# Kernel optimization log

Hardware: AMD Instinct MI355X
Metric: run time of the kernel (lower is better)

The kernel has to match this reference:

```python
import math
import jax, jax.numpy as jnp
import numpy as np

DIM = 1024
N_HEADS = 16
N_KV_HEADS = 4
HEAD_DIM = 64
WINDOW = 512
EPS = 1e-6
B, S = 2, 2048

def _alibi_slopes(n_heads):
    def pow2(n):
        r = 2.0 ** (-8.0 / n)
        return np.array([r ** (i + 1) for i in range(n)], dtype=np.float32)
    if math.log2(n_heads).is_integer():
        return pow2(n_heads)
    m = 2 ** math.floor(math.log2(n_heads))
    return np.concatenate([pow2(m), pow2(2 * m)[::2][: n_heads - m]])

def _rmsnorm(x, w, eps=EPS):
    var = jnp.mean(x * x, axis=-1, keepdims=True)
    return x * jax.lax.rsqrt(var + eps) * w

def setup_inputs() -> dict:
    key = jax.random.key(0)
    ks = jax.random.split(key, 8)
    x = jax.random.normal(ks[0], (B, S, DIM), dtype=jnp.float32)
    wq = 0.02 * jax.random.normal(ks[1], (N_HEADS * HEAD_DIM, DIM), dtype=jnp.float32)
    wk = 0.02 * jax.random.normal(ks[2], (N_KV_HEADS * HEAD_DIM, DIM), dtype=jnp.float32)
    wv = 0.02 * jax.random.normal(ks[3], (N_KV_HEADS * HEAD_DIM, DIM), dtype=jnp.float32)
    wo = 0.02 * jax.random.normal(ks[4], (DIM, N_HEADS * HEAD_DIM), dtype=jnp.float32)
    q_norm_w = jnp.ones((N_HEADS * HEAD_DIM,), dtype=jnp.float32)
    k_norm_w = jnp.ones((N_KV_HEADS * HEAD_DIM,), dtype=jnp.float32)
    return {"x": x, "wq": wq, "wk": wk, "wv": wv, "wo": wo,
            "q_norm_w": q_norm_w, "k_norm_w": k_norm_w}

def reference(x, wq, wk, wv, wo, q_norm_w, k_norm_w):
    bsz, seqlen, _ = x.shape
    repeats = N_HEADS // N_KV_HEADS
    xq = _rmsnorm(x @ wq.T, q_norm_w)
    xk = _rmsnorm(x @ wk.T, k_norm_w)
    xv = x @ wv.T
    # [b, h, s, d]
    q = xq.reshape(bsz, seqlen, N_HEADS, HEAD_DIM).transpose(0, 2, 1, 3)
    k = xk.reshape(bsz, seqlen, N_KV_HEADS, HEAD_DIM).transpose(0, 2, 1, 3)
    v = xv.reshape(bsz, seqlen, N_KV_HEADS, HEAD_DIM).transpose(0, 2, 1, 3)
    k = jnp.repeat(k, repeats, axis=1)
    v = jnp.repeat(v, repeats, axis=1)
    pos = jnp.arange(seqlen)
    rel = pos[None, :] - pos[:, None]  # [s_q, s_k], key - query
    slopes = jnp.asarray(_alibi_slopes(N_HEADS))
    bias = slopes[:, None, None] * rel[None].astype(x.dtype)  # [h, s, s]
    masked = (rel > 0) | (rel < -WINDOW)  # causal + sliding window
    bias = jnp.where(masked[None], -jnp.inf, bias)
    scale = 1.0 / math.sqrt(HEAD_DIM)
    scores = jnp.einsum('bhqd,bhkd->bhqk', q, k) * scale + bias[None]
    probs = jax.nn.softmax(scores, axis=-1)
    y = jnp.einsum('bhqk,bhkd->bhqd', probs, v)
    y = y.transpose(0, 2, 1, 3).reshape(bsz, seqlen, N_HEADS * HEAD_DIM)
    return y @ wo.T
```

## Files before the change

kernel.cpp:

```cpp
#include <hip/hip_runtime.h>

typedef unsigned short u16;
typedef unsigned int u32;

typedef __bf16 bf16x8 __attribute__((ext_vector_type(8)));
typedef float f32x4 __attribute__((ext_vector_type(4)));

__device__ __forceinline__ u16 f2bf(float f) {
  __bf16 h = (__bf16)f;
  return __builtin_bit_cast(u16, h);
}
__device__ __forceinline__ u32 pk2bf(float a, float b) {
  __bf16 lo = (__bf16)a, hi = (__bf16)b;
  return (u32)__builtin_bit_cast(u16, lo) | ((u32)__builtin_bit_cast(u16, hi) << 16);
}
__device__ __forceinline__ float bf2f(u16 v) {
  u32 u = (u32)v << 16;
  return __builtin_bit_cast(float, u);
}

typedef const __attribute__((address_space(1))) u32 gbl_u32;
typedef __attribute__((address_space(3))) u32 lds_u32;
__device__ __forceinline__ void gload_lds16(const u16* g, u16* l) {
  __builtin_amdgcn_global_load_lds((gbl_u32*)g, (lds_u32*)l, 16, 0, 0);
}

__global__ __launch_bounds__(256)
void cvt_all_kernel(const float* __restrict__ x, const float* __restrict__ wq,
                    const float* __restrict__ wk, const float* __restrict__ wv,
                    const float* __restrict__ wo, u16* __restrict__ x_bf,
                    u16* __restrict__ wcat_bf, u16* __restrict__ wo_bf) {
  int t = blockIdx.x * 256 + threadIdx.x;
  const float* src;
  u16* dst;
  if (t < 1048576) {
    src = x; dst = x_bf;
  } else if (t < 1310720) {
    src = wq; dst = wcat_bf; t -= 1048576;
  } else if (t < 1376256) {
    src = wk; dst = wcat_bf + 1048576; t -= 1310720;
  } else if (t < 1441792) {
    src = wv; dst = wcat_bf + 1310720; t -= 1376256;
  } else {
    src = wo; dst = wo_bf; t -= 1441792;
  }
  const int i = t * 4;
  float4 v = *(const float4*)(src + i);
  uint2 p;
  p.x = pk2bf(v.x, v.y);
  p.y = pk2bf(v.z, v.w);
  *(uint2*)(dst + i) = p;
}

template <typename OutT>
__global__ __launch_bounds__(256)
void gemm_bt_kernel(const u16* __restrict__ A, const u16* __restrict__ B,
                    OutT* __restrict__ C, int M, int N, int K) {
  __shared__ u16 As[2][64 * 64];
  __shared__ u16 Bs[2][128 * 64];
  const int tid = threadIdx.x;
  const int lane = tid & 63;
  const int wave = tid >> 6;
  const int wm = (wave >> 1) * 32;
  const int wn = (wave & 1) * 64;
  const int l15 = lane & 15;
  const int quad = lane >> 4;
  const int sw = l15 & 7;
  const size_t bm = (size_t)blockIdx.y * 64;
  const size_t bn = (size_t)blockIdx.x * 128;

  f32x4 acc[2][4];
#pragma unroll
  for (int i = 0; i < 2; ++i)
#pragma unroll
    for (int j = 0; j < 4; ++j) acc[i][j] = f32x4{0.f, 0.f, 0.f, 0.f};

  const int r0 = tid >> 3;
  const int bswz = ((tid & 7) ^ (r0 & 7)) * 8;
  const u16* gA0 = A + (bm + r0) * (size_t)K + bswz;
  const u16* gA1 = A + (bm + r0 + 32) * (size_t)K + bswz;
  const u16* gB0 = B + (bn + r0) * (size_t)K + bswz;
  const u16* gB1 = B + (bn + r0 + 32) * (size_t)K + bswz;
  const u16* gB2 = B + (bn + r0 + 64) * (size_t)K + bswz;
  const u16* gB3 = B + (bn + r0 + 96) * (size_t)K + bswz;

#define STAGE(bufi, kk)                                   \
  do {                                                    \
    gload_lds16(gA0 + (kk), &As[bufi][tid * 8]);          \
    gload_lds16(gA1 + (kk), &As[bufi][2048 + tid * 8]);   \
    gload_lds16(gB0 + (kk), &Bs[bufi][tid * 8]);          \
    gload_lds16(gB1 + (kk), &Bs[bufi][2048 + tid * 8]);   \
    gload_lds16(gB2 + (kk), &Bs[bufi][4096 + tid * 8]);   \
    gload_lds16(gB3 + (kk), &Bs[bufi][6144 + tid * 8]);   \
  } while (0)

  STAGE(0, 0);
  int buf = 0;
  for (int k0 = 0; k0 < K; k0 += 64) {
    __syncthreads();
    if (k0 + 64 < K) STAGE(buf ^ 1, k0 + 64);
    const u16* as = As[buf];
    const u16* bs = Bs[buf];
#pragma unroll
    for (int h = 0; h < 2; ++h) {
      const int cb = quad + 4 * h;
      bf16x8 af[2], bfr[4];
#pragma unroll
      for (int i = 0; i < 2; ++i)
        af[i] = *(const bf16x8*)(&as[(wm + i * 16 + l15) * 64 + ((cb ^ sw) * 8)]);
#pragma unroll
      for (int j = 0; j < 4; ++j)
        bfr[j] = *(const bf16x8*)(&bs[(wn + j * 16 + l15) * 64 + ((cb ^ sw) * 8)]);
#pragma unroll
      for (int i = 0; i < 2; ++i)
#pragma unroll
        for (int j = 0; j < 4; ++j)
          acc[i][j] = __builtin_amdgcn_mfma_f32_16x16x32_bf16(af[i], bfr[j], acc[i][j], 0, 0, 0);
    }
    buf ^= 1;
  }
#undef STAGE

  const int rq = quad * 4;
#pragma unroll
  for (int i = 0; i < 2; ++i) {
#pragma unroll
    for (int r = 0; r < 4; ++r) {
      OutT* crow = C + (bm + wm + i * 16 + rq + r) * (size_t)N + bn + wn + l15;
#pragma unroll
      for (int j = 0; j < 4; ++j) {
        if constexpr (sizeof(OutT) == 2)
          crow[j * 16] = f2bf(acc[i][j][r]);
        else
          crow[j * 16] = acc[i][j][r];
      }
    }
  }
}

__global__ __launch_bounds__(256)
void norm_vtrans_kernel(u16* __restrict__ qkv, const float* __restrict__ qw,
                        const float* __restrict__ kw, u16* __restrict__ vt) {
  __shared__ u16 shmem[64 * 72];
  const int bid = blockIdx.x;
  const int tid = threadIdx.x;
  if (bid < 4096) {
    float* red = (float*)shmem;
    u16* row = qkv + (size_t)bid * 1536;
    uint2 pk = *(const uint2*)(row + tid * 4);
    float v0 = bf2f((u16)pk.x), v1 = bf2f((u16)(pk.x >> 16));
    float v2 = bf2f((u16)pk.y), v3 = bf2f((u16)(pk.y >> 16));
    float ss = v0 * v0 + v1 * v1 + v2 * v2 + v3 * v3;
#pragma unroll
    for (int off = 32; off > 0; off >>= 1) ss += __shfl_down(ss, off);
    if ((tid & 63) == 0) red[tid >> 6] = ss;
    __syncthreads();
    float tot = red[0] + red[1] + red[2] + red[3];
    float rn = rsqrtf(tot * (1.0f / 1024.0f) + 1e-6f);
    float4 w = *(const float4*)(qw + tid * 4);
    uint2 po;
    po.x = pk2bf(v0 * rn * w.x, v1 * rn * w.y);
    po.y = pk2bf(v2 * rn * w.z, v3 * rn * w.w);
    *(uint2*)(row + tid * 4) = po;
    if (tid < 64) {
      uint2 kp = *(const uint2*)(row + 1024 + tid * 4);
      float k0 = bf2f((u16)kp.x), k1 = bf2f((u16)(kp.x >> 16));
      float k2 = bf2f((u16)kp.y), k3 = bf2f((u16)(kp.y >> 16));
      float sk = k0 * k0 + k1 * k1 + k2 * k2 + k3 * k3;
#pragma unroll
      for (int off = 32; off > 0; off >>= 1) sk += __shfl_down(sk, off);
      float tk = __shfl(sk, 0);
      float rk = rsqrtf(tk * (1.0f / 256.0f) + 1e-6f);
      float4 w2 = *(const float4*)(kw + tid * 4);
      uint2 ko;
      ko.x = pk2bf(k0 * rk * w2.x, k1 * rk * w2.y);
      ko.y = pk2bf(k2 * rk * w2.z, k3 * rk * w2.w);
      *(uint2*)(row + 1024 + tid * 4) = ko;
    }
  } else {
    const int e = bid - 4096;
    const int t0 = (e & 31) * 64, kvh = (e >> 5) & 3, b = e >> 7;
    u16(*tile)[72] = (u16(*)[72])shmem;
    const int r = tid >> 2, c16 = (tid & 3) * 16;
    const u16* src = qkv + (size_t)(b * 2048 + t0 + r) * 1536 + 1280 + kvh * 64 + c16;
    *(uint4*)&tile[r][c16] = *(const uint4*)src;
    *(uint4*)&tile[r][c16 + 8] = *(const uint4*)(src + 8);
    __syncthreads();
    const int d = tid >> 2, t16 = (tid & 3) * 16;
    u16 o[16];
#pragma unroll
    for (int j = 0; j < 16; ++j) o[j] = tile[t16 + j][d];
    u16* dst = vt + (size_t)((b * 4 + kvh) * 64 + d) * 2048 + t0 + t16;
    *(uint4*)dst = *(uint4*)&o[0];
    *(uint4*)(dst + 8) = *(uint4*)&o[8];
  }
}

__global__ __launch_bounds__(512)
void attn_kernel(const u16* __restrict__ qkvbf, const u16* __restrict__ vt,
                 u16* __restrict__ ybf) {
  __shared__ u16 Ks[2][64 * 64];
  __shared__ u16 Vts[2][64 * 64];
  __shared__ u16 Ps[128 * 72];
  const int qt = blockIdx.x, h = blockIdx.y, b = blockIdx.z;
  const int kvh = h >> 2, q0 = qt * 128;
  const int tid = threadIdx.x, lane = tid & 63, w = tid >> 6;
  const int l15 = lane & 15, quad = lane >> 4;
  const int swl = l15 & 7;

  const u16* qrow = qkvbf + (size_t)(b * 2048 + q0 + w * 16 + l15) * 1536 + h * 64 + quad * 8;
  const bf16x8 qf0 = *(const bf16x8*)qrow;
  const bf16x8 qf1 = *(const bf16x8*)(qrow + 32);

  const int sr = tid >> 3;
  const int bswz = ((tid & 7) ^ (sr & 7)) * 8;
  const u16* kg = qkvbf + (size_t)(b * 2048 + sr) * 1536 + 1024 + kvh * 64 + bswz;
  const u16* vg = vt + (size_t)((b * 4 + kvh) * 64 + sr) * 2048 + bswz;

#define ASTAGE(bufi, cc)                                          \
  do {                                                            \
    gload_lds16(kg + (size_t)(cc) * 1536, &Ks[bufi][tid * 8]);    \
    gload_lds16(vg + (cc), &Vts[bufi][tid * 8]);                  \
  } while (0)

  f32x4 O[4];
#pragma unroll
  for (int jd = 0; jd < 4; ++jd) O[jd] = f32x4{0.f, 0.f, 0.f, 0.f};
  float m_i = -1e30f, l_i = 0.f;
  const float LOG2E = 1.44269504f;
  const float sc2 = 0.125f * LOG2E;
  const float slope2 = exp2f(-0.5f * (float)(h + 1)) * LOG2E;
  const int c_lo = (q0 >= 512) ? (q0 - 512) : 0;
  const int c_hi = q0 + 64;
  const int myq_lo = q0 + w * 16;
  const int myq_hi = myq_lo + 15;
  const int myq = myq_lo + l15;
  const float srr1 = slope2, srr2 = slope2 * 2.0f, srr3 = slope2 * 3.0f;
  const float si16 = slope2 * 16.0f;

  ASTAGE(0, c_lo);
  int buf = 0;

  for (int c = c_lo; c <= c_hi; c += 64) {
    __syncthreads();
    if (c + 64 <= c_hi) ASTAGE(buf ^ 1, c + 64);

    if (!(c > myq_hi || c + 63 < myq_lo - 512)) {
      f32x4 st[4];
      __builtin_amdgcn_s_setprio(1);
#pragma unroll
      for (int i = 0; i < 4; ++i) {
        const int ro = (i * 16 + l15) * 64;
        bf16x8 a0 = *(const bf16x8*)&Ks[buf][ro + ((quad ^ swl) * 8)];
        bf16x8 a1 = *(const bf16x8*)&Ks[buf][ro + (((4 + quad) ^ swl) * 8)];
        f32x4 z = f32x4{0.f, 0.f, 0.f, 0.f};
        z = __builtin_amdgcn_mfma_f32_16x16x32_bf16(a0, qf0, z, 0, 0, 0);
        st[i] = __builtin_amdgcn_mfma_f32_16x16x32_bf16(a1, qf1, z, 0, 0, 0);
      }
      __builtin_amdgcn_s_setprio(0);

      float sv[4][4];
      float rm = -1e30f;
      const bool interior = (c + 63 <= myq_lo) && (c + 512 >= myq_hi);
      if (interior) {
        float bi = slope2 * (float)(c + quad * 4 - myq);
#pragma unroll
        for (int i = 0; i < 4; ++i) {
          float v0 = fmaf(st[i][0], sc2, bi);
          float v1 = fmaf(st[i][1], sc2, bi + srr1);
          float v2 = fmaf(st[i][2], sc2, bi + srr2);
          float v3 = fmaf(st[i][3], sc2, bi + srr3);
          sv[i][0] = v0; sv[i][1] = v1; sv[i][2] = v2; sv[i][3] = v3;
          rm = fmaxf(fmaxf(fmaxf(rm, v0), fmaxf(v1, v2)), v3);
          bi += si16;
        }
      } else {
#pragma unroll
        for (int i = 0; i < 4; ++i)
#pragma unroll
          for (int r = 0; r < 4; ++r) {
            const int key = c + i * 16 + quad * 4 + r;
            const int rel = key - myq;
            float val = (rel > 0 || rel < -512) ? -1e30f
                                                : fmaf(st[i][r], sc2, slope2 * (float)rel);
            sv[i][r] = val;
            rm = fmaxf(rm, val);
          }
      }
      rm = fmaxf(rm, __shfl_xor(rm, 16));
      rm = fmaxf(rm, __shfl_xor(rm, 32));
      const float mn = fmaxf(m_i, rm);
      const float alpha = exp2f(m_i - mn);
      float ls = 0.f;
#pragma unroll
      for (int i = 0; i < 4; ++i) {
        float p0 = exp2f(sv[i][0] - mn);
        float p1 = exp2f(sv[i][1] - mn);
        float p2 = exp2f(sv[i][2] - mn);
        float p3 = exp2f(sv[i][3] - mn);
        ls += (p0 + p1) + (p2 + p3);
        uint2 pw;
        pw.x = pk2bf(p0, p1);
        pw.y = pk2bf(p2, p3);
        *(uint2*)&Ps[(w * 16 + l15) * 72 + i * 16 + quad * 4] = pw;
      }
      ls += __shfl_xor(ls, 16);
      ls += __shfl_xor(ls, 32);
      l_i = l_i * alpha + ls;
      m_i = mn;

      float ar[4];
#pragma unroll
      for (int r = 0; r < 4; ++r) ar[r] = __shfl(alpha, quad * 4 + r);
#pragma unroll
      for (int jd = 0; jd < 4; ++jd)
#pragma unroll
        for (int r = 0; r < 4; ++r) O[jd][r] *= ar[r];

      bf16x8 pf0 = *(const bf16x8*)&Ps[(w * 16 + l15) * 72 + quad * 8];
      bf16x8 pf1 = *(const bf16x8*)&Ps[(w * 16 + l15) * 72 + 32 + quad * 8];
      __builtin_amdgcn_s_setprio(1);
#pragma unroll
      for (int jd = 0; jd < 4; ++jd) {
        const int ro = (jd * 16 + l15) * 64;
        bf16x8 v0 = *(const bf16x8*)&Vts[buf][ro + ((quad ^ swl) * 8)];
        bf16x8 v1 = *(const bf16x8*)&Vts[buf][ro + (((4 + quad) ^ swl) * 8)];
        O[jd] = __builtin_amdgcn_mfma_f32_16x16x32_bf16(pf0, v0, O[jd], 0, 0, 0);
        O[jd] = __builtin_amdgcn_mfma_f32_16x16x32_bf16(pf1, v1, O[jd], 0, 0, 0);
      }
      __builtin_amdgcn_s_setprio(0);
    }
    buf ^= 1;
  }
#undef ASTAGE

  float lr[4];
#pragma unroll
  for (int r = 0; r < 4; ++r) lr[r] = __shfl(l_i, quad * 4 + r);
#pragma unroll
  for (int r = 0; r < 4; ++r) {
    const float inv = 1.0f / lr[r];
    u16* orow = ybf + (size_t)(b * 2048 + q0 + w * 16 + quad * 4 + r) * 1024 + h * 64 + l15;
#pragma unroll
    for (int jd = 0; jd < 4; ++jd) orow[jd * 16] = f2bf(O[jd][r] * inv);
  }
}

extern "C" void kernel_launch(void* const* d_in, const int* in_sizes, int n_in,
                              void* d_out, int out_size, void* d_ws, size_t ws_size,
                              hipStream_t stream) {
  const float* x = (const float*)d_in[0];
  const float* wq = (const float*)d_in[1];
  const float* wk = (const float*)d_in[2];
  const float* wv = (const float*)d_in[3];
  const float* wo = (const float*)d_in[4];
  const float* qnw = (const float*)d_in[5];
  const float* knw = (const float*)d_in[6];
  float* out = (float*)d_out;
  char* ws = (char*)d_ws;

  u16* x_bf = (u16*)(ws);
  u16* wcat_bf = (u16*)(ws + 8388608);
  u16* wo_bf = (u16*)(ws + 11534336);
  u16* qkv_bf = (u16*)(ws + 13631488);
  u16* vt_bf = (u16*)(ws + 26214400);
  u16* y_bf = (u16*)(ws + 28311552);

  cvt_all_kernel<<<6656, 256, 0, stream>>>(x, wq, wk, wv, wo, x_bf, wcat_bf, wo_bf);

  gemm_bt_kernel<u16><<<dim3(12, 64), 256, 0, stream>>>(x_bf, wcat_bf, qkv_bf, 4096, 1536, 1024);
  norm_vtrans_kernel<<<4352, 256, 0, stream>>>(qkv_bf, qnw, knw, vt_bf);
  attn_kernel<<<dim3(16, 16, 2), 512, 0, stream>>>(qkv_bf, vt_bf, y_bf);
  gemm_bt_kernel<float><<<dim3(8, 64), 256, 0, stream>>>(y_bf, wo_bf, out, 4096, 1024, 1024);
}
```

Baseline: 155.0 us.

## Use a 128x128 single-buffered GEMM tile for the QKV projection

Adds a new GEMM kernel that computes a 128x128 output tile per block, with each wave owning a 64x64 sub-tile, and uses it for the QKV projection in place of the 64x128 double-buffered kernel. Larger tiles raise operand reuse from shared memory and halve the number of blocks. The new kernel gives up double buffering: it loads, synchronizes, then computes each K-step, so global-load latency is no longer overlapped, and the 384 blocks may underfill the GPU's CUs. The other edits are variable renames with no effect.

```diff
diff --git a/kernel.cpp b/kernel.cpp
--- a/kernel.cpp
+++ b/kernel.cpp
@@ -54,6 +54,86 @@
 
 template <typename OutT>
 __global__ __launch_bounds__(256)
+void gemm128_kernel(const u16* __restrict__ A, const u16* __restrict__ B,
+                    OutT* __restrict__ C, int N, int K) {
+  __shared__ u16 As[128 * 64];
+  __shared__ u16 Bs[128 * 64];
+  const int tid = threadIdx.x;
+  const int lane = tid & 63;
+  const int wave = tid >> 6;
+  const int wm = (wave & 1) * 64;
+  const int wn = (wave >> 1) * 64;
+  const int l15 = lane & 15;
+  const int quad = lane >> 4;
+  const int sw = l15 & 7;
+  const size_t bm = (size_t)blockIdx.y * 128;
+  const size_t bn = (size_t)blockIdx.x * 128;
+
+  f32x4 acc[4][4];
+#pragma unroll
+  for (int i = 0; i < 4; ++i)
+#pragma unroll
+    for (int j = 0; j < 4; ++j) acc[i][j] = f32x4{0.f, 0.f, 0.f, 0.f};
+
+  const int r0 = tid >> 3;
+  const int bswz = ((tid & 7) ^ (r0 & 7)) * 8;
+  const u16* gA0 = A + (bm + r0) * (size_t)K + bswz;
+  const u16* gA1 = A + (bm + r0 + 32) * (size_t)K + bswz;
+  const u16* gA2 = A + (bm + r0 + 64) * (size_t)K + bswz;
+  const u16* gA3 = A + (bm + r0 + 96) * (size_t)K + bswz;
+  const u16* gB0 = B + (bn + r0) * (size_t)K + bswz;
+  const u16* gB1 = B + (bn + r0 + 32) * (size_t)K + bswz;
+  const u16* gB2 = B + (bn + r0 + 64) * (size_t)K + bswz;
+  const u16* gB3 = B + (bn + r0 + 96) * (size_t)K + bswz;
+
+  for (int k0 = 0; k0 < K; k0 += 64) {
+    __syncthreads();
+    gload_lds16(gA0 + k0, &As[tid * 8]);
+    gload_lds16(gA1 + k0, &As[2048 + tid * 8]);
+    gload_lds16(gA2 + k0, &As[4096 + tid * 8]);
+    gload_lds16(gA3 + k0, &As[6144 + tid * 8]);
+    gload_lds16(gB0 + k0, &Bs[tid * 8]);
+    gload_lds16(gB1 + k0, &Bs[2048 + tid * 8]);
+    gload_lds16(gB2 + k0, &Bs[4096 + tid * 8]);
+    gload_lds16(gB3 + k0, &Bs[6144 + tid * 8]);
+    __syncthreads();
+#pragma unroll
+    for (int h = 0; h < 2; ++h) {
+      const int cb = quad + 4 * h;
+      bf16x8 af[4], bfr[4];
+#pragma unroll
+      for (int i = 0; i < 4; ++i)
+        af[i] = *(const bf16x8*)(&As[(wm + i * 16 + l15) * 64 + ((cb ^ sw) * 8)]);
+#pragma unroll
+      for (int j = 0; j < 4; ++j)
+        bfr[j] = *(const bf16x8*)(&Bs[(wn + j * 16 + l15) * 64 + ((cb ^ sw) * 8)]);
+#pragma unroll
+      for (int i = 0; i < 4; ++i)
+#pragma unroll
+        for (int j = 0; j < 4; ++j)
+          acc[i][j] = __builtin_amdgcn_mfma_f32_16x16x32_bf16(af[i], bfr[j], acc[i][j], 0, 0, 0);
+    }
+  }
+
+  const int rq = quad * 4;
+#pragma unroll
+  for (int i = 0; i < 4; ++i) {
+#pragma unroll
+    for (int r = 0; r < 4; ++r) {
+      OutT* crow = C + (bm + wm + i * 16 + rq + r) * (size_t)N + bn + wn + l15;
+#pragma unroll
+      for (int j = 0; j < 4; ++j) {
+        if constexpr (sizeof(OutT) == 2)
+          crow[j * 16] = f2bf(acc[i][j][r]);
+        else
+          crow[j * 16] = acc[i][j][r];
+      }
+    }
+  }
+}
+
+template <typename OutT>
+__global__ __launch_bounds__(256)
 void gemm_bt_kernel(const u16* __restrict__ A, const u16* __restrict__ B,
                     OutT* __restrict__ C, int M, int N, int K) {
   __shared__ u16 As[2][64 * 64];
@@ -84,21 +164,21 @@
   const u16* gB2 = B + (bn + r0 + 64) * (size_t)K + bswz;
   const u16* gB3 = B + (bn + r0 + 96) * (size_t)K + bswz;
 
-#define STAGE(bufi, kk)                                   \
-  do {                                                    \
-    gload_lds16(gA0 + (kk), &As[bufi][tid * 8]);          \
-    gload_lds16(gA1 + (kk), &As[bufi][2048 + tid * 8]);   \
-    gload_lds16(gB0 + (kk), &Bs[bufi][tid * 8]);          \
-    gload_lds16(gB1 + (kk), &Bs[bufi][2048 + tid * 8]);   \
-    gload_lds16(gB2 + (kk), &Bs[bufi][4096 + tid * 8]);   \
-    gload_lds16(gB3 + (kk), &Bs[bufi][6144 + tid * 8]);   \
+#define FSTAGE(bufi, kk)                                    \
+  do {                                                      \
+    gload_lds16(gA0 + (kk), &As[bufi][tid * 8]);            \
+    gload_lds16(gA1 + (kk), &As[bufi][2048 + tid * 8]);     \
+    gload_lds16(gB0 + (kk), &Bs[bufi][tid * 8]);            \
+    gload_lds16(gB1 + (kk), &Bs[bufi][2048 + tid * 8]);     \
+    gload_lds16(gB2 + (kk), &Bs[bufi][4096 + tid * 8]);     \
+    gload_lds16(gB3 + (kk), &Bs[bufi][6144 + tid * 8]);     \
   } while (0)
 
-  STAGE(0, 0);
+  FSTAGE(0, 0);
   int buf = 0;
   for (int k0 = 0; k0 < K; k0 += 64) {
     __syncthreads();
-    if (k0 + 64 < K) STAGE(buf ^ 1, k0 + 64);
+    if (k0 + 64 < K) FSTAGE(buf ^ 1, k0 + 64);
     const u16* as = As[buf];
     const u16* bs = Bs[buf];
 #pragma unroll
@@ -119,7 +199,7 @@
     }
     buf ^= 1;
   }
-#undef STAGE
+#undef FSTAGE
 
   const int rq = quad * 4;
 #pragma unroll
@@ -266,12 +346,12 @@
         float bi = slope2 * (float)(c + quad * 4 - myq);
 #pragma unroll
         for (int i = 0; i < 4; ++i) {
-          float v0 = fmaf(st[i][0], sc2, bi);
-          float v1 = fmaf(st[i][1], sc2, bi + srr1);
-          float v2 = fmaf(st[i][2], sc2, bi + srr2);
-          float v3 = fmaf(st[i][3], sc2, bi + srr3);
-          sv[i][0] = v0; sv[i][1] = v1; sv[i][2] = v2; sv[i][3] = v3;
-          rm = fmaxf(fmaxf(fmaxf(rm, v0), fmaxf(v1, v2)), v3);
+          float x0 = fmaf(st[i][0], sc2, bi);
+          float x1 = fmaf(st[i][1], sc2, bi + srr1);
+          float x2 = fmaf(st[i][2], sc2, bi + srr2);
+          float x3 = fmaf(st[i][3], sc2, bi + srr3);
+          sv[i][0] = x0; sv[i][1] = x1; sv[i][2] = x2; sv[i][3] = x3;
+          rm = fmaxf(fmaxf(fmaxf(rm, x0), fmaxf(x1, x2)), x3);
           bi += si16;
         }
       } else {
@@ -368,7 +448,7 @@
 
   cvt_all_kernel<<<6656, 256, 0, stream>>>(x, wq, wk, wv, wo, x_bf, wcat_bf, wo_bf);
 
-  gemm_bt_kernel<u16><<<dim3(12, 64), 256, 0, stream>>>(x_bf, wcat_bf, qkv_bf, 4096, 1536, 1024);
+  gemm128_kernel<u16><<<dim3(12, 32), 256, 0, stream>>>(x_bf, wcat_bf, qkv_bf, 1536, 1024);
   norm_vtrans_kernel<<<4352, 256, 0, stream>>>(qkv_bf, qnw, knw, vt_bf);
   attn_kernel<<<dim3(16, 16, 2), 512, 0, stream>>>(qkv_bf, vt_bf, y_bf);
   gemm_bt_kernel<float><<<dim3(8, 64), 256, 0, stream>>>(y_bf, wo_bf, out, 4096, 1024, 1024);
```

New measurement: 159.5 us. 1.03x slower.

## Use one wave per row in QK norm and lazily rescale softmax accumulator

Applied to the files above, without the earlier changes.

The norm kernel now handles four rows per block, one wavefront per row, with 16 elements per lane. This removes the LDS reduction and block barrier and cuts the grid from 4352 to 1280 blocks. In attention, the running max is updated and the output accumulator rescaled only when some lane's new max exceeds the old one by more than 8 (log2 units), which skips the exp and the multiplies in most iterations. The lazy rescale lets probabilities reach up to 2^8 before normalization, a bounded range that fits within bf16 and fp32.

```diff
diff --git a/kernel.cpp b/kernel.cpp
--- a/kernel.cpp
+++ b/kernel.cpp
@@ -84,21 +84,21 @@
   const u16* gB2 = B + (bn + r0 + 64) * (size_t)K + bswz;
   const u16* gB3 = B + (bn + r0 + 96) * (size_t)K + bswz;
 
-#define STAGE(bufi, kk)                                   \
-  do {                                                    \
-    gload_lds16(gA0 + (kk), &As[bufi][tid * 8]);          \
-    gload_lds16(gA1 + (kk), &As[bufi][2048 + tid * 8]);   \
-    gload_lds16(gB0 + (kk), &Bs[bufi][tid * 8]);          \
-    gload_lds16(gB1 + (kk), &Bs[bufi][2048 + tid * 8]);   \
-    gload_lds16(gB2 + (kk), &Bs[bufi][4096 + tid * 8]);   \
-    gload_lds16(gB3 + (kk), &Bs[bufi][6144 + tid * 8]);   \
+#define FSTAGE(bufi, kk)                                    \
+  do {                                                      \
+    gload_lds16(gA0 + (kk), &As[bufi][tid * 8]);            \
+    gload_lds16(gA1 + (kk), &As[bufi][2048 + tid * 8]);     \
+    gload_lds16(gB0 + (kk), &Bs[bufi][tid * 8]);            \
+    gload_lds16(gB1 + (kk), &Bs[bufi][2048 + tid * 8]);     \
+    gload_lds16(gB2 + (kk), &Bs[bufi][4096 + tid * 8]);     \
+    gload_lds16(gB3 + (kk), &Bs[bufi][6144 + tid * 8]);     \
   } while (0)
 
-  STAGE(0, 0);
+  FSTAGE(0, 0);
   int buf = 0;
   for (int k0 = 0; k0 < K; k0 += 64) {
     __syncthreads();
-    if (k0 + 64 < K) STAGE(buf ^ 1, k0 + 64);
+    if (k0 + 64 < K) FSTAGE(buf ^ 1, k0 + 64);
     const u16* as = As[buf];
     const u16* bs = Bs[buf];
 #pragma unroll
@@ -119,7 +119,7 @@
     }
     buf ^= 1;
   }
-#undef STAGE
+#undef FSTAGE
 
   const int rq = quad * 4;
 #pragma unroll
@@ -141,44 +141,60 @@
 __global__ __launch_bounds__(256)
 void norm_vtrans_kernel(u16* __restrict__ qkv, const float* __restrict__ qw,
                         const float* __restrict__ kw, u16* __restrict__ vt) {
-  __shared__ u16 shmem[64 * 72];
   const int bid = blockIdx.x;
   const int tid = threadIdx.x;
-  if (bid < 4096) {
-    float* red = (float*)shmem;
-    u16* row = qkv + (size_t)bid * 1536;
-    uint2 pk = *(const uint2*)(row + tid * 4);
-    float v0 = bf2f((u16)pk.x), v1 = bf2f((u16)(pk.x >> 16));
-    float v2 = bf2f((u16)pk.y), v3 = bf2f((u16)(pk.y >> 16));
-    float ss = v0 * v0 + v1 * v1 + v2 * v2 + v3 * v3;
-#pragma unroll
-    for (int off = 32; off > 0; off >>= 1) ss += __shfl_down(ss, off);
-    if ((tid & 63) == 0) red[tid >> 6] = ss;
-    __syncthreads();
-    float tot = red[0] + red[1] + red[2] + red[3];
-    float rn = rsqrtf(tot * (1.0f / 1024.0f) + 1e-6f);
-    float4 w = *(const float4*)(qw + tid * 4);
-    uint2 po;
-    po.x = pk2bf(v0 * rn * w.x, v1 * rn * w.y);
-    po.y = pk2bf(v2 * rn * w.z, v3 * rn * w.w);
-    *(uint2*)(row + tid * 4) = po;
-    if (tid < 64) {
-      uint2 kp = *(const uint2*)(row + 1024 + tid * 4);
-      float k0 = bf2f((u16)kp.x), k1 = bf2f((u16)(kp.x >> 16));
-      float k2 = bf2f((u16)kp.y), k3 = bf2f((u16)(kp.y >> 16));
-      float sk = k0 * k0 + k1 * k1 + k2 * k2 + k3 * k3;
-#pragma unroll
-      for (int off = 32; off > 0; off >>= 1) sk += __shfl_down(sk, off);
-      float tk = __shfl(sk, 0);
-      float rk = rsqrtf(tk * (1.0f / 256.0f) + 1e-6f);
-      float4 w2 = *(const float4*)(kw + tid * 4);
-      uint2 ko;
-      ko.x = pk2bf(k0 * rk * w2.x, k1 * rk * w2.y);
-      ko.y = pk2bf(k2 * rk * w2.z, k3 * rk * w2.w);
-      *(uint2*)(row + 1024 + tid * 4) = ko;
-    }
+  if (bid < 1024) {
+    const int lane = tid & 63, wv = tid >> 6;
+    u16* rp = qkv + (size_t)(bid * 4 + wv) * 1536;
+    uint4 qa = *(const uint4*)(rp + lane * 16);
+    uint4 qb = *(const uint4*)(rp + lane * 16 + 8);
+    uint2 kp = *(const uint2*)(rp + 1024 + lane * 4);
+    float qv[16];
+    const u32* pa = (const u32*)&qa;
+    const u32* pb = (const u32*)&qb;
+#pragma unroll
+    for (int j = 0; j < 4; ++j) {
+      qv[2 * j] = bf2f((u16)pa[j]);
+      qv[2 * j + 1] = bf2f((u16)(pa[j] >> 16));
+      qv[8 + 2 * j] = bf2f((u16)pb[j]);
+      qv[9 + 2 * j] = bf2f((u16)(pb[j] >> 16));
+    }
+    float k0 = bf2f((u16)kp.x), k1 = bf2f((u16)(kp.x >> 16));
+    float k2 = bf2f((u16)kp.y), k3 = bf2f((u16)(kp.y >> 16));
+    float ss = 0.f;
+#pragma unroll
+    for (int j = 0; j < 16; ++j) ss = fmaf(qv[j], qv[j], ss);
+    float sk = k0 * k0 + k1 * k1 + k2 * k2 + k3 * k3;
+#pragma unroll
+    for (int off = 1; off < 64; off <<= 1) {
+      ss += __shfl_xor(ss, off);
+      sk += __shfl_xor(sk, off);
+    }
+    const float rn = rsqrtf(ss * (1.0f / 1024.0f) + 1e-6f);
+    const float rk = rsqrtf(sk * (1.0f / 256.0f) + 1e-6f);
+    float4 w0 = *(const float4*)(qw + lane * 16);
+    float4 w1 = *(const float4*)(qw + lane * 16 + 4);
+    float4 w2 = *(const float4*)(qw + lane * 16 + 8);
+    float4 w3 = *(const float4*)(qw + lane * 16 + 12);
+    uint4 o1, o2;
+    o1.x = pk2bf(qv[0] * rn * w0.x, qv[1] * rn * w0.y);
+    o1.y = pk2bf(qv[2] * rn * w0.z, qv[3] * rn * w0.w);
+    o1.z = pk2bf(qv[4] * rn * w1.x, qv[5] * rn * w1.y);
+    o1.w = pk2bf(qv[6] * rn * w1.z, qv[7] * rn * w1.w);
+    o2.x = pk2bf(qv[8] * rn * w2.x, qv[9] * rn * w2.y);
+    o2.y = pk2bf(qv[10] * rn * w2.z, qv[11] * rn * w2.w);
+    o2.z = pk2bf(qv[12] * rn * w3.x, qv[13] * rn * w3.y);
+    o2.w = pk2bf(qv[14] * rn * w3.z, qv[15] * rn * w3.w);
+    *(uint4*)(rp + lane * 16) = o1;
+    *(uint4*)(rp + lane * 16 + 8) = o2;
+    float4 wk4 = *(const float4*)(kw + lane * 4);
+    uint2 ko;
+    ko.x = pk2bf(k0 * rk * wk4.x, k1 * rk * wk4.y);
+    ko.y = pk2bf(k2 * rk * wk4.z, k3 * rk * wk4.w);
+    *(uint2*)(rp + 1024 + lane * 4) = ko;
   } else {
-    const int e = bid - 4096;
+    __shared__ u16 shmem[64 * 72];
+    const int e = bid - 1024;
     const int t0 = (e & 31) * 64, kvh = (e >> 5) & 3, b = e >> 7;
     u16(*tile)[72] = (u16(*)[72])shmem;
     const int r = tid >> 2, c16 = (tid & 3) * 16;
@@ -266,12 +282,12 @@
         float bi = slope2 * (float)(c + quad * 4 - myq);
 #pragma unroll
         for (int i = 0; i < 4; ++i) {
-          float v0 = fmaf(st[i][0], sc2, bi);
-          float v1 = fmaf(st[i][1], sc2, bi + srr1);
-          float v2 = fmaf(st[i][2], sc2, bi + srr2);
-          float v3 = fmaf(st[i][3], sc2, bi + srr3);
-          sv[i][0] = v0; sv[i][1] = v1; sv[i][2] = v2; sv[i][3] = v3;
-          rm = fmaxf(fmaxf(fmaxf(rm, v0), fmaxf(v1, v2)), v3);
+          float x0 = fmaf(st[i][0], sc2, bi);
+          float x1 = fmaf(st[i][1], sc2, bi + srr1);
+          float x2 = fmaf(st[i][2], sc2, bi + srr2);
+          float x3 = fmaf(st[i][3], sc2, bi + srr3);
+          sv[i][0] = x0; sv[i][1] = x1; sv[i][2] = x2; sv[i][3] = x3;
+          rm = fmaxf(fmaxf(fmaxf(rm, x0), fmaxf(x1, x2)), x3);
           bi += si16;
         }
       } else {
@@ -289,8 +305,9 @@
       }
       rm = fmaxf(rm, __shfl_xor(rm, 16));
       rm = fmaxf(rm, __shfl_xor(rm, 32));
-      const float mn = fmaxf(m_i, rm);
-      const float alpha = exp2f(m_i - mn);
+      const bool nskip = !__all(rm <= m_i + 8.0f);
+      float mn = m_i;
+      if (nskip) mn = fmaxf(m_i, rm);
       float ls = 0.f;
 #pragma unroll
       for (int i = 0; i < 4; ++i) {
@@ -306,16 +323,19 @@
       }
       ls += __shfl_xor(ls, 16);
       ls += __shfl_xor(ls, 32);
-      l_i = l_i * alpha + ls;
-      m_i = mn;
-
-      float ar[4];
-#pragma unroll
-      for (int r = 0; r < 4; ++r) ar[r] = __shfl(alpha, quad * 4 + r);
-#pragma unroll
-      for (int jd = 0; jd < 4; ++jd)
-#pragma unroll
-        for (int r = 0; r < 4; ++r) O[jd][r] *= ar[r];
+      if (nskip) {
+        const float alpha = exp2f(m_i - mn);
+        l_i *= alpha;
+        m_i = mn;
+        float ar[4];
+#pragma unroll
+        for (int r = 0; r < 4; ++r) ar[r] = __shfl(alpha, quad * 4 + r);
+#pragma unroll
+        for (int jd = 0; jd < 4; ++jd)
+#pragma unroll
+          for (int r = 0; r < 4; ++r) O[jd][r] *= ar[r];
+      }
+      l_i += ls;
 
       bf16x8 pf0 = *(const bf16x8*)&Ps[(w * 16 + l15) * 72 + quad * 8];
       bf16x8 pf1 = *(const bf16x8*)&Ps[(w * 16 + l15) * 72 + 32 + quad * 8];
@@ -369,7 +389,7 @@
   cvt_all_kernel<<<6656, 256, 0, stream>>>(x, wq, wk, wv, wo, x_bf, wcat_bf, wo_bf);
 
   gemm_bt_kernel<u16><<<dim3(12, 64), 256, 0, stream>>>(x_bf, wcat_bf, qkv_bf, 4096, 1536, 1024);
-  norm_vtrans_kernel<<<4352, 256, 0, stream>>>(qkv_bf, qnw, knw, vt_bf);
+  norm_vtrans_kernel<<<1280, 256, 0, stream>>>(qkv_bf, qnw, knw, vt_bf);
   attn_kernel<<<dim3(16, 16, 2), 512, 0, stream>>>(qkv_bf, vt_bf, y_bf);
   gemm_bt_kernel<float><<<dim3(8, 64), 256, 0, stream>>>(y_bf, wo_bf, out, 4096, 1024, 1024);
 }
```

Result: no change. 154.3 us (median of 3 runs) (-0.4%).
